# Optimization experiments

Measured on AMD Instinct MI355X. Metric: run time of the kernel, lower is better.

The kernel has to match this reference:

```python
import math
import jax, jax.numpy as jnp
import numpy as np

N = 512; E_EDGES = 16384; NODE_DIM = 64; HID = 128; FF = 2048; VOCAB = 50; L = 2; H = 8; SEQ = 100


def setup_inputs() -> dict:
    key = jax.random.key(0)
    ks = jax.random.split(key, 24)
    s = 0.02
    rn = lambda k, shape: jax.random.normal(k, shape, jnp.float32) * s
    return {
        "x": jax.random.normal(ks[0], (N, NODE_DIM), jnp.float32),
        "edge_index": jax.random.randint(ks[1], (2, E_EDGES), 0, N, dtype=jnp.int32),
        "gcn1_w": rn(ks[2], (NODE_DIM, HID)), "gcn1_b": rn(ks[3], (HID,)),
        "gcn2_w": rn(ks[4], (HID, HID)),     "gcn2_b": rn(ks[5], (HID,)),
        "fc_w":   rn(ks[6], (HID, HID)),     "fc_b":   rn(ks[7], (HID,)),
        # decoder: per layer, 4 proj mats (q,k,v,out) for self-attn and cross-attn
        "sa_w": rn(ks[8], (L, 4, HID, HID)), "sa_b": rn(ks[9], (L, 4, HID)),
        "ca_w": rn(ks[10], (L, 4, HID, HID)), "ca_b": rn(ks[11], (L, 4, HID)),
        "ln_w": jnp.ones((L, 3, HID), jnp.float32), "ln_b": jnp.zeros((L, 3, HID), jnp.float32),
        "ff_w1": rn(ks[12], (L, HID, FF)), "ff_b1": rn(ks[13], (L, FF)),
        "ff_w2": rn(ks[14], (L, FF, HID)), "ff_b2": rn(ks[15], (L, HID)),
        "out_w": rn(ks[16], (HID, VOCAB)), "out_b": rn(ks[17], (VOCAB,)),
    }


def _gcn(x, W, b, src, dst, n):
    # PyG GCNConv: add self-loops, symmetric norm, aggregate source->target
    h = x @ W                                   # [N, out]
    loop = jnp.arange(n, dtype=src.dtype)
    s = jnp.concatenate([src, loop])
    d = jnp.concatenate([dst, loop])
    deg = jax.ops.segment_sum(jnp.ones_like(d, x.dtype), d, num_segments=n)
    dinv = jax.lax.rsqrt(deg)                   # deg >= 1 thanks to self-loops
    norm = dinv[s] * dinv[d]                    # [E+N]
    return jax.ops.segment_sum(h[s] * norm[:, None], d, num_segments=n) + b


def _layernorm(x, w, b, eps=1e-5):
    m = x.mean(-1, keepdims=True)
    v = ((x - m) ** 2).mean(-1, keepdims=True)
    return (x - m) * jax.lax.rsqrt(v + eps) * w + b


def _mha(q_in, kv_in, w, b):
    # q_in [S,Nb,E], kv_in [T,Nb,E]; w [4,E,E] (q,k,v,out), b [4,E]
    S, Nb, E = q_in.shape
    T = kv_in.shape[0]
    Dh = E // H
    q = (q_in @ w[0] + b[0]).reshape(S, Nb, H, Dh)
    k = (kv_in @ w[1] + b[1]).reshape(T, Nb, H, Dh)
    v = (kv_in @ w[2] + b[2]).reshape(T, Nb, H, Dh)
    att = jnp.einsum('snhd,tnhd->nhst', q, k) / math.sqrt(Dh)
    p = jax.nn.softmax(att, axis=-1)
    o = jnp.einsum('nhst,tnhd->snhd', p, v).reshape(S, Nb, E)
    return o @ w[3] + b[3]


def _forward(x, edge_index, gcn1_w, gcn1_b, gcn2_w, gcn2_b, fc_w, fc_b,
             sa_w, sa_b, ca_w, ca_b, ln_w, ln_b, ff_w1, ff_b1, ff_w2, ff_b2,
             out_w, out_b):
    n = x.shape[0]
    src, dst = edge_index[0], edge_index[1]
    # quantum_embedding: rz = (cos(phi)-sin(phi)) * (cos(theta)*x + sin(theta)*tanh(x))
    qx = (math.cos(0.05) - math.sin(0.05)) * (math.cos(0.1) * x + math.sin(0.1) * jnp.tanh(x))
    h = jax.nn.relu(_gcn(qx, gcn1_w, gcn1_b, src, dst, n))
    h = jax.nn.relu(_gcn(h, gcn2_w, gcn2_b, src, dst, n))
    h = h @ fc_w + fc_b                          # [N, HID]
    mem = h[None]                                # [1, N, HID] (memory, seq-first)
    tgt = jnp.zeros((SEQ, n, h.shape[1]), h.dtype)
    for l in range(L):                           # post-norm TransformerDecoderLayer
        tgt = _layernorm(tgt + _mha(tgt, tgt, sa_w[l], sa_b[l]), ln_w[l, 0], ln_b[l, 0])
        tgt = _layernorm(tgt + _mha(tgt, mem, ca_w[l], ca_b[l]), ln_w[l, 1], ln_b[l, 1])
        f = jax.nn.relu(tgt @ ff_w1[l] + ff_b1[l]) @ ff_w2[l] + ff_b2[l]
        tgt = _layernorm(tgt + f, ln_w[l, 2], ln_b[l, 2])
    return tgt @ out_w + out_b                   # [SEQ, N, VOCAB]


def reference(x, edge_index, gcn1_w, gcn1_b, gcn2_w, gcn2_b, fc_w, fc_b,
              sa_w, sa_b, ca_w, ca_b, ln_w, ln_b, ff_w1, ff_b1, ff_w2, ff_b2,
              out_w, out_b):
    return _forward(x, edge_index, gcn1_w, gcn1_b, gcn2_w, gcn2_b, fc_w, fc_b,
                    sa_w, sa_b, ca_w, ca_b, ln_w, ln_b, ff_w1, ff_b1, ff_w2, ff_b2,
                    out_w, out_b)
```

## Files before the change

kernel.cpp:

```cpp
#include <hip/hip_runtime.h>
#include <math.h>

#define NN      512
#define EE      16384
#define NDIM    64
#define HID     128
#define FFD     2048
#define VOCAB   50
#define SEQ     100

#define QA 0.94877109112428797f
#define QB 0.99500416527802582f
#define QC 0.099833416646828155f


struct BArgs {
    const int* ei; int* cnt;
    const float* x; const float* g1w; float* pre1;
    const float* A[3]; const float* ab[3]; const float* Bm[3]; const float* bb[3];
    float* outM[3];
    const float* ab3; const float* B3; const float* bb3; float* out3;
};

__global__ void k_b(BArgs a) {
    int B = blockIdx.x, t = threadIdx.x;
    if (B < 64) {
        int e = B * 256 + t;
        atomicAdd(&a.cnt[a.ei[EE + e]], 1);
        return;
    }
    if (B < 320) {
        __shared__ float qxs[2][NDIM];
        int q = B - 64;
        int row0 = q * 2;
        if (t < 2 * NDIM) {
            float v = a.x[row0 * NDIM + t];
            qxs[t >> 6][t & 63] = QA * (QB * v + QC * tanhf(v));
        }
        __syncthreads();
        int r = t >> 7, col = t & 127;
        float acc = 0.0f;
#pragma unroll 8
        for (int k = 0; k < NDIM; k++) acc = fmaf(qxs[r][k], a.g1w[k * HID + col], acc);
        a.pre1[(row0 + r) * HID + col] = acc;
        return;
    }
    if (B < 320 + 195) {
        int q = B - 320;
        int jm = q / 65;
        int i = (q - jm * 65) * 256 + t;
        if (i >= 129 * HID) return;
        int rw = i >> 7, col = i & 127;
        const float* Bm = a.Bm[jm];
        float acc;
        if (rw < 128) {
            const float* ar = a.A[jm] + rw * HID;
            acc = 0.0f;
#pragma unroll 8
            for (int k = 0; k < HID; k++) acc = fmaf(ar[k], Bm[k * HID + col], acc);
        } else {
            acc = a.bb[jm][col];
#pragma unroll 8
            for (int k = 0; k < HID; k++) acc = fmaf(a.ab[jm][k], Bm[k * HID + col], acc);
        }
        a.outM[jm][i] = acc;
        return;
    }
    if (t < HID) {
        float acc = a.bb3[t];
#pragma unroll 8
        for (int k = 0; k < HID; k++) acc = fmaf(a.ab3[k], a.B3[k * HID + t], acc);
        a.out3[t] = acc;
    }
}


struct CArgs {
    const int* cnt; int* offs; int* cursor; float* dinv;
    const float* fcw; const float* fcb;
    const float* Mca0; const float* Mca1; float* Mfc0; float* Mfc1;
};

__global__ void k_c(CArgs a) {
    int B = blockIdx.x, t = threadIdx.x;
    if (B == 0) {
        __shared__ int sh[512];
        int c0 = a.cnt[t], c1 = a.cnt[t + 256];
        sh[t] = c0; sh[t + 256] = c1;
        __syncthreads();
        for (int o = 1; o < 512; o <<= 1) {
            int x0 = (t >= o) ? sh[t - o] : 0;
            int x1 = (t + 256 >= o) ? sh[t + 256 - o] : 0;
            __syncthreads();
            sh[t] += x0; sh[t + 256] += x1;
            __syncthreads();
        }
        a.offs[t + 1] = sh[t];
        a.offs[t + 257] = sh[t + 256];
        if (t == 0) a.offs[0] = 0;
        a.cursor[t] = sh[t] - c0;
        a.cursor[t + 256] = sh[t + 256] - c1;
        a.dinv[t] = rsqrtf((float)c0 + 1.0f);
        a.dinv[t + 256] = rsqrtf((float)c1 + 1.0f);
        return;
    }
    int q = B - 1;
    int jm = q / 65;
    int i = (q - jm * 65) * 256 + t;
    if (i >= 129 * HID) return;
    int rw = i >> 7, col = i & 127;
    const float* M = jm ? a.Mca1 : a.Mca0;
    float* o = jm ? a.Mfc1 : a.Mfc0;
    float acc;
    if (rw < 128) {
        const float* ar = a.fcw + rw * HID;
        acc = 0.0f;
#pragma unroll 8
        for (int k = 0; k < HID; k++) acc = fmaf(ar[k], M[k * HID + col], acc);
    } else {
        acc = M[128 * HID + col];
#pragma unroll 8
        for (int k = 0; k < HID; k++) acc = fmaf(a.fcb[k], M[k * HID + col], acc);
    }
    o[i] = acc;
}


__global__ void k_scatter(const int* __restrict__ ei, int* __restrict__ cursor,
                          int* __restrict__ csr) {
    int e = blockIdx.x * 256 + threadIdx.x;
    if (e < EE) {
        int d = ei[EE + e];
        int slot = atomicAdd(&cursor[d], 1);
        csr[slot] = ei[e];
    }
}


__device__ __forceinline__ float gather_row(const float* __restrict__ pre,
                                            const float* __restrict__ dinv,
                                            const int* __restrict__ offs,
                                            const int* __restrict__ csr,
                                            int row, int j) {
    float dd = dinv[row];
    float acc = pre[row * HID + j] * dd;
    int i = offs[row], e = offs[row + 1];
    for (; i + 3 < e; i += 4) {
        int s0 = csr[i], s1 = csr[i + 1], s2 = csr[i + 2], s3 = csr[i + 3];
        float a0 = pre[s0 * HID + j] * dinv[s0];
        float a1 = pre[s1 * HID + j] * dinv[s1];
        float a2 = pre[s2 * HID + j] * dinv[s2];
        float a3 = pre[s3 * HID + j] * dinv[s3];
        acc += (a0 + a1) + (a2 + a3);
    }
    for (; i < e; ++i) {
        int s = csr[i];
        acc += pre[s * HID + j] * dinv[s];
    }
    return acc * dd;
}

__device__ __forceinline__ float rowln(float v, float w, float b, float* sh, int t) {
    int r = t >> 7;
    float s1 = v, s2 = v * v;
#pragma unroll
    for (int o = 32; o > 0; o >>= 1) {
        s1 += __shfl_down(s1, o);
        s2 += __shfl_down(s2, o);
    }
    int wv = (t >> 6) & 1;
    if ((t & 63) == 0) { sh[r * 4 + wv] = s1; sh[r * 4 + 2 + wv] = s2; }
    __syncthreads();
    float mean = (sh[r * 4] + sh[r * 4 + 1]) * (1.0f / HID);
    float m2   = (sh[r * 4 + 2] + sh[r * 4 + 3]) * (1.0f / HID);
    float rstd = rsqrtf(m2 - mean * mean + 1e-5f);
    float out = (v - mean) * rstd * w + b;
    __syncthreads();
    return out;
}


__global__ void k_gather_mm(const float* __restrict__ pre1, const float* __restrict__ dinv,
                            const int* __restrict__ offs, const int* __restrict__ csr,
                            const float* __restrict__ g1b, const float* __restrict__ g2w,
                            float* __restrict__ pre2) {
    __shared__ float sh_h[2][HID];
    int t = threadIdx.x, j = t & 127, r = t >> 7;
    int row = blockIdx.x * 2 + r;
    float g = gather_row(pre1, dinv, offs, csr, row, j);
    sh_h[r][j] = fmaxf(g + g1b[j], 0.0f);
    __syncthreads();
    float acc = 0.0f;
#pragma unroll 8
    for (int k = 0; k < HID; k++) acc = fmaf(sh_h[r][k], g2w[k * HID + j], acc);
    pre2[row * HID + j] = acc;
}


__global__ void k_row0(const float* __restrict__ pre2, const float* __restrict__ dinv,
                       const int* __restrict__ offs, const int* __restrict__ csr,
                       const float* __restrict__ g2b,
                       const float* __restrict__ Mfc0, const float* __restrict__ Mfc1,
                       const float* __restrict__ sa0bias,
                       const float* __restrict__ ln0w, const float* __restrict__ ln0b,
                       const float* __restrict__ ln1w, const float* __restrict__ ln1b,
                       float* __restrict__ ca1out, float* __restrict__ t0out) {
    __shared__ float sh_h[2][HID];
    __shared__ float shln[8];
    int t = threadIdx.x, j = t & 127, r = t >> 7;
    int row = blockIdx.x * 2 + r;
    float g = gather_row(pre2, dinv, offs, csr, row, j);
    sh_h[r][j] = fmaxf(g + g2b[j], 0.0f);
    __syncthreads();
    float a0 = Mfc0[128 * HID + j], a1 = Mfc1[128 * HID + j];
#pragma unroll 4
    for (int k = 0; k < HID; k++) {
        float hk = sh_h[r][k];
        a0 = fmaf(hk, Mfc0[k * HID + j], a0);
        a1 = fmaf(hk, Mfc1[k * HID + j], a1);
    }
    ca1out[row * HID + j] = a1;
    float v = rowln(sa0bias[j], ln0w[j], ln0b[j], shln, t);
    v = rowln(v + a0, ln1w[j], ln1b[j], shln, t);
    t0out[row * HID + j] = v;
}


__global__ __launch_bounds__(512)
void k_fff(const float* __restrict__ tin, const float* __restrict__ W1,
           const float* __restrict__ b1, const float* __restrict__ W2,
           float* __restrict__ part) {
    __shared__ float sh_t[16][HID];
    __shared__ float sh_m[16][256];
    int t = threadIdx.x;
    int kc = blockIdx.x & 7, rg = blockIdx.x >> 3;
    int row0 = rg * 16, c0 = kc * 256;

    {
        const float4* tp = (const float4*)(tin + row0 * HID);
        float4 v = tp[t];
        *(float4*)&sh_t[t >> 5][(t & 31) * 4] = v;
    }
    __syncthreads();

    {
        int rg2  = t >> 6;
        int col4 = (t & 63) * 4;
        float4 bias = *(const float4*)&b1[c0 + col4];
        float a00 = bias.x, a01 = bias.y, a02 = bias.z, a03 = bias.w;
        float a10 = bias.x, a11 = bias.y, a12 = bias.z, a13 = bias.w;
        const float* w1p = W1 + c0 + col4;
        const float* x0 = sh_t[2 * rg2];
        const float* x1 = sh_t[2 * rg2 + 1];
#pragma unroll 8
        for (int k = 0; k < HID; k++) {
            float4 w = *(const float4*)&w1p[k * FFD];
            float s0 = x0[k], s1 = x1[k];
            a00 = fmaf(s0, w.x, a00); a01 = fmaf(s0, w.y, a01);
            a02 = fmaf(s0, w.z, a02); a03 = fmaf(s0, w.w, a03);
            a10 = fmaf(s1, w.x, a10); a11 = fmaf(s1, w.y, a11);
            a12 = fmaf(s1, w.z, a12); a13 = fmaf(s1, w.w, a13);
        }
        float4 m0, m1;
        m0.x = fmaxf(a00, 0.f); m0.y = fmaxf(a01, 0.f);
        m0.z = fmaxf(a02, 0.f); m0.w = fmaxf(a03, 0.f);
        m1.x = fmaxf(a10, 0.f); m1.y = fmaxf(a11, 0.f);
        m1.z = fmaxf(a12, 0.f); m1.w = fmaxf(a13, 0.f);
        *(float4*)&sh_m[2 * rg2][col4]     = m0;
        *(float4*)&sh_m[2 * rg2 + 1][col4] = m1;
    }
    __syncthreads();

    {
        int rowg = t >> 5;
        int col4 = (t & 31) * 4;
        float a0 = 0.f, a1 = 0.f, a2 = 0.f, a3 = 0.f;
        const float* w2p = W2 + c0 * HID + col4;
        const float* mp = sh_m[rowg];
#pragma unroll 8
        for (int kk = 0; kk < 256; kk++) {
            float4 w = *(const float4*)&w2p[kk * HID];
            float m = mp[kk];
            a0 = fmaf(m, w.x, a0); a1 = fmaf(m, w.y, a1);
            a2 = fmaf(m, w.z, a2); a3 = fmaf(m, w.w, a3);
        }
        float4 o; o.x = a0; o.y = a1; o.z = a2; o.w = a3;
        *(float4*)&part[kc * (NN * HID) + (row0 + rowg) * HID + col4] = o;
    }
}


__global__ void k_row1(const float* __restrict__ part, const float* __restrict__ fb2,
                       const float* __restrict__ t0, const float* __restrict__ Msa1,
                       const float* __restrict__ ca1,
                       const float* __restrict__ ln2w, const float* __restrict__ ln2b,
                       const float* __restrict__ ln3w, const float* __restrict__ ln3b,
                       const float* __restrict__ ln4w, const float* __restrict__ ln4b,
                       float* __restrict__ t2out) {
    __shared__ float sh_t1[2][HID];
    __shared__ float shln[8];
    int t = threadIdx.x, j = t & 127, r = t >> 7;
    int row = blockIdx.x * 2 + r;
    float v = fb2[j] + t0[row * HID + j];
#pragma unroll
    for (int s = 0; s < 8; s++) v += part[s * (NN * HID) + row * HID + j];
    v = rowln(v, ln2w[j], ln2b[j], shln, t);
    sh_t1[r][j] = v;
    __syncthreads();
    float s1 = Msa1[128 * HID + j];
#pragma unroll 8
    for (int k = 0; k < HID; k++) s1 = fmaf(sh_t1[r][k], Msa1[k * HID + j], s1);
    float u = rowln(v + s1, ln3w[j], ln3b[j], shln, t);
    u = rowln(u + ca1[row * HID + j], ln4w[j], ln4b[j], shln, t);
    t2out[row * HID + j] = u;
}


__global__ void k_rowout(const float* __restrict__ part, const float* __restrict__ fb2,
                         const float* __restrict__ t2,
                         const float* __restrict__ ln5w, const float* __restrict__ ln5b,
                         const float* __restrict__ ow, const float* __restrict__ ob,
                         float* __restrict__ out) {
    __shared__ float sh3[2][HID];
    __shared__ float shln[8];
    __shared__ __align__(16) float sh_lg[100];
    int t = threadIdx.x, j = t & 127, r = t >> 7;
    int row = blockIdx.x * 2 + r;
    float v = fb2[j] + t2[row * HID + j];
#pragma unroll
    for (int s = 0; s < 8; s++) v += part[s * (NN * HID) + row * HID + j];
    v = rowln(v, ln5w[j], ln5b[j], shln, t);
    sh3[r][j] = v;
    __syncthreads();
    if (j < VOCAB) {
        float acc = ob[j];
#pragma unroll 8
        for (int k = 0; k < HID; k++) acc = fmaf(sh3[r][k], ow[k * VOCAB + j], acc);
        sh_lg[r * VOCAB + j] = acc;
    }
    __syncthreads();
    int base = blockIdx.x * (2 * VOCAB);
    for (int idx = t; idx < SEQ * 25; idx += 256) {
        int s = idx / 25, p4 = (idx - s * 25) * 4;
        *(float4*)&out[s * (NN * VOCAB) + base + p4] = *(const float4*)&sh_lg[p4];
    }
}


extern "C" void kernel_launch(void* const* d_in, const int* in_sizes, int n_in,
                              void* d_out, int out_size, void* d_ws, size_t ws_size,
                              hipStream_t stream) {
    (void)in_sizes; (void)n_in; (void)out_size; (void)ws_size;
    const float* x   = (const float*)d_in[0];
    const int*   ei  = (const int*)d_in[1];
    const float* g1w = (const float*)d_in[2];
    const float* g1b = (const float*)d_in[3];
    const float* g2w = (const float*)d_in[4];
    const float* g2b = (const float*)d_in[5];
    const float* fcw = (const float*)d_in[6];
    const float* fcb = (const float*)d_in[7];
    const float* saw = (const float*)d_in[8];
    const float* sab = (const float*)d_in[9];
    const float* caw = (const float*)d_in[10];
    const float* cab = (const float*)d_in[11];
    const float* lnw = (const float*)d_in[12];
    const float* lnb = (const float*)d_in[13];
    const float* fw1 = (const float*)d_in[14];
    const float* fb1 = (const float*)d_in[15];
    const float* fw2 = (const float*)d_in[16];
    const float* fb2 = (const float*)d_in[17];
    const float* ow  = (const float*)d_in[18];
    const float* ob  = (const float*)d_in[19];
    float* out = (float*)d_out;

    float* ws      = (float*)d_ws;
    float* pre1    = ws;
    float* pre2    = ws + 65536;
    float* t0      = ws + 131072;
    float* t2      = ws + 196608;
    float* ca1     = ws + 262144;
    float* Msa1    = ws + 327680;
    float* Mca0    = ws + 344192;
    float* Mca1    = ws + 360704;
    float* Mfc0    = ws + 377216;
    float* Mfc1    = ws + 393728;
    float* sa0bias = ws + 410240;
    float* dinv    = ws + 410368;
    int*   cnt     = (int*)(ws + 410880);
    int*   offs    = cnt + 512;
    int*   cursor  = offs + 516;
    int*   csr     = cursor + 512;
    float* part    = ws + 429056;

    hipMemsetAsync(cnt, 0, 512 * sizeof(int), stream);

    {
        BArgs a;
        a.ei = ei; a.cnt = cnt; a.x = x; a.g1w = g1w; a.pre1 = pre1;
        a.A[0]  = saw + (4 + 2) * HID * HID;  a.ab[0] = sab + (4 + 2) * HID;
        a.Bm[0] = saw + (4 + 3) * HID * HID;  a.bb[0] = sab + (4 + 3) * HID;
        a.outM[0] = Msa1;
        a.A[1]  = caw + 2 * HID * HID;        a.ab[1] = cab + 2 * HID;
        a.Bm[1] = caw + 3 * HID * HID;        a.bb[1] = cab + 3 * HID;
        a.outM[1] = Mca0;
        a.A[2]  = caw + (4 + 2) * HID * HID;  a.ab[2] = cab + (4 + 2) * HID;
        a.Bm[2] = caw + (4 + 3) * HID * HID;  a.bb[2] = cab + (4 + 3) * HID;
        a.outM[2] = Mca1;
        a.ab3 = sab + 2 * HID;  a.B3 = saw + 3 * HID * HID;  a.bb3 = sab + 3 * HID;
        a.out3 = sa0bias;
        k_b<<<516, 256, 0, stream>>>(a);
    }

    {
        CArgs a;
        a.cnt = cnt; a.offs = offs; a.cursor = cursor; a.dinv = dinv;
        a.fcw = fcw; a.fcb = fcb;
        a.Mca0 = Mca0; a.Mca1 = Mca1; a.Mfc0 = Mfc0; a.Mfc1 = Mfc1;
        k_c<<<131, 256, 0, stream>>>(a);
    }

    k_scatter<<<64, 256, 0, stream>>>(ei, cursor, csr);

    k_gather_mm<<<256, 256, 0, stream>>>(pre1, dinv, offs, csr, g1b, g2w, pre2);

    k_row0<<<256, 256, 0, stream>>>(pre2, dinv, offs, csr, g2b, Mfc0, Mfc1, sa0bias,
                                    lnw + 0 * HID, lnb + 0 * HID,
                                    lnw + 1 * HID, lnb + 1 * HID, ca1, t0);

    k_fff<<<256, 512, 0, stream>>>(t0, fw1, fb1, fw2, part);

    k_row1<<<256, 256, 0, stream>>>(part, fb2, t0, Msa1, ca1,
                                    lnw + 2 * HID, lnb + 2 * HID,
                                    lnw + 3 * HID, lnb + 3 * HID,
                                    lnw + 4 * HID, lnb + 4 * HID, t2);

    k_fff<<<256, 512, 0, stream>>>(t2, fw1 + HID * FFD, fb1 + FFD, fw2 + FFD * HID, part);

    k_rowout<<<256, 256, 0, stream>>>(part, fb2 + HID, t2,
                                      lnw + 5 * HID, lnb + 5 * HID, ow, ob, out);
}
```

Baseline: 120.2 us.

## Halve FFN block row tile and split second GEMM K across thread halves

The fused FFN kernel now processes 8 rows per block instead of 16 and launches twice as many blocks. Each thread computes one row in the first GEMM. In the second GEMM the 256-wide K chunk is split between the two thread halves, which are then reduced through shared memory. This raises parallelism and block count on a many-CU GPU, at the cost of reading weights twice as often across blocks and adding an extra barrier.

```diff
diff --git a/kernel.cpp b/kernel.cpp
--- a/kernel.cpp
+++ b/kernel.cpp
@@ -230,13 +230,13 @@
 void k_fff(const float* __restrict__ tin, const float* __restrict__ W1,
            const float* __restrict__ b1, const float* __restrict__ W2,
            float* __restrict__ part) {
-    __shared__ float sh_t[16][HID];
-    __shared__ float sh_m[16][256];
+    __shared__ float sh_t[8][HID];
+    __shared__ float sh_m[8][256];
     int t = threadIdx.x;
     int kc = blockIdx.x & 7, rg = blockIdx.x >> 3;
-    int row0 = rg * 16, c0 = kc * 256;
-
-    {
+    int row0 = rg * 8, c0 = kc * 256;
+
+    if (t < 256) {
         const float4* tp = (const float4*)(tin + row0 * HID);
         float4 v = tp[t];
         *(float4*)&sh_t[t >> 5][(t & 31) * 4] = v;
@@ -244,48 +244,51 @@
     __syncthreads();
 
     {
-        int rg2  = t >> 6;
+        int row  = t >> 6;
         int col4 = (t & 63) * 4;
         float4 bias = *(const float4*)&b1[c0 + col4];
-        float a00 = bias.x, a01 = bias.y, a02 = bias.z, a03 = bias.w;
-        float a10 = bias.x, a11 = bias.y, a12 = bias.z, a13 = bias.w;
+        float a0 = bias.x, a1 = bias.y, a2 = bias.z, a3 = bias.w;
         const float* w1p = W1 + c0 + col4;
-        const float* x0 = sh_t[2 * rg2];
-        const float* x1 = sh_t[2 * rg2 + 1];
+        const float* xr = sh_t[row];
 #pragma unroll 8
         for (int k = 0; k < HID; k++) {
             float4 w = *(const float4*)&w1p[k * FFD];
-            float s0 = x0[k], s1 = x1[k];
-            a00 = fmaf(s0, w.x, a00); a01 = fmaf(s0, w.y, a01);
-            a02 = fmaf(s0, w.z, a02); a03 = fmaf(s0, w.w, a03);
-            a10 = fmaf(s1, w.x, a10); a11 = fmaf(s1, w.y, a11);
-            a12 = fmaf(s1, w.z, a12); a13 = fmaf(s1, w.w, a13);
-        }
-        float4 m0, m1;
-        m0.x = fmaxf(a00, 0.f); m0.y = fmaxf(a01, 0.f);
-        m0.z = fmaxf(a02, 0.f); m0.w = fmaxf(a03, 0.f);
-        m1.x = fmaxf(a10, 0.f); m1.y = fmaxf(a11, 0.f);
-        m1.z = fmaxf(a12, 0.f); m1.w = fmaxf(a13, 0.f);
-        *(float4*)&sh_m[2 * rg2][col4]     = m0;
-        *(float4*)&sh_m[2 * rg2 + 1][col4] = m1;
+            float s = xr[k];
+            a0 = fmaf(s, w.x, a0); a1 = fmaf(s, w.y, a1);
+            a2 = fmaf(s, w.z, a2); a3 = fmaf(s, w.w, a3);
+        }
+        float4 m;
+        m.x = fmaxf(a0, 0.f); m.y = fmaxf(a1, 0.f);
+        m.z = fmaxf(a2, 0.f); m.w = fmaxf(a3, 0.f);
+        *(float4*)&sh_m[row][col4] = m;
     }
     __syncthreads();
 
     {
-        int rowg = t >> 5;
         int col4 = (t & 31) * 4;
+        int row  = (t >> 5) & 7;
+        int kh   = t >> 8;
         float a0 = 0.f, a1 = 0.f, a2 = 0.f, a3 = 0.f;
-        const float* w2p = W2 + c0 * HID + col4;
-        const float* mp = sh_m[rowg];
-#pragma unroll 8
-        for (int kk = 0; kk < 256; kk++) {
+        const float* w2p = W2 + (c0 + kh * 128) * HID + col4;
+        const float* mp = &sh_m[row][kh * 128];
+#pragma unroll 8
+        for (int kk = 0; kk < 128; kk++) {
             float4 w = *(const float4*)&w2p[kk * HID];
             float m = mp[kk];
             a0 = fmaf(m, w.x, a0); a1 = fmaf(m, w.y, a1);
             a2 = fmaf(m, w.z, a2); a3 = fmaf(m, w.w, a3);
         }
-        float4 o; o.x = a0; o.y = a1; o.z = a2; o.w = a3;
-        *(float4*)&part[kc * (NN * HID) + (row0 + rowg) * HID + col4] = o;
+        float* shred = &sh_t[0][0];
+        if (kh) {
+            float4 r; r.x = a0; r.y = a1; r.z = a2; r.w = a3;
+            *(float4*)&shred[(t - 256) * 4] = r;
+        }
+        __syncthreads();
+        if (!kh) {
+            float4 o = *(float4*)&shred[t * 4];
+            o.x += a0; o.y += a1; o.z += a2; o.w += a3;
+            *(float4*)&part[kc * (NN * HID) + (row0 + row) * HID + col4] = o;
+        }
     }
 }
 
@@ -427,14 +430,14 @@
                                     lnw + 0 * HID, lnb + 0 * HID,
                                     lnw + 1 * HID, lnb + 1 * HID, ca1, t0);
 
-    k_fff<<<256, 512, 0, stream>>>(t0, fw1, fb1, fw2, part);
+    k_fff<<<512, 512, 0, stream>>>(t0, fw1, fb1, fw2, part);
 
     k_row1<<<256, 256, 0, stream>>>(part, fb2, t0, Msa1, ca1,
                                     lnw + 2 * HID, lnb + 2 * HID,
                                     lnw + 3 * HID, lnb + 3 * HID,
                                     lnw + 4 * HID, lnb + 4 * HID, t2);
 
-    k_fff<<<256, 512, 0, stream>>>(t2, fw1 + HID * FFD, fb1 + FFD, fw2 + FFD * HID, part);
+    k_fff<<<512, 512, 0, stream>>>(t2, fw1 + HID * FFD, fb1 + FFD, fw2 + FFD * HID, part);
 
     k_rowout<<<256, 256, 0, stream>>>(part, fb2 + HID, t2,
                                       lnw + 5 * HID, lnb + 5 * HID, ow, ob, out);
```

After: 134.0 us. 1.11x slower.

## Fuse all stages into one cooperative persistent kernel with grid syncs

Applied to the files above, without the earlier changes.

Replaces the eight separate kernel launches with a single cooperative kernel of 256 blocks × 512 threads that separates stages with grid.sync(). Row-wise stages now process 4 rows per block instead of 2, and the pre-stages are re-partitioned to match the larger blocks. The goal is to remove per-launch overhead and the inter-kernel drain gaps, which matter at this small problem size. In exchange it adds grid-wide barrier costs, and several stages leave many blocks idle.

```diff
diff --git a/kernel.cpp b/kernel.cpp
--- a/kernel.cpp
+++ b/kernel.cpp
@@ -1,5 +1,8 @@
 #include <hip/hip_runtime.h>
+#include <hip/hip_cooperative_groups.h>
 #include <math.h>
+
+namespace cg = cooperative_groups;
 
 #define NN      512
 #define EE      16384
@@ -13,128 +16,22 @@
 #define QB 0.99500416527802582f
 #define QC 0.099833416646828155f
 
-
-struct BArgs {
-    const int* ei; int* cnt;
-    const float* x; const float* g1w; float* pre1;
-    const float* A[3]; const float* ab[3]; const float* Bm[3]; const float* bb[3];
-    float* outM[3];
-    const float* ab3; const float* B3; const float* bb3; float* out3;
+struct GArgs {
+    const int* ei;
+    const float* x; const float* g1w; const float* g1b;
+    const float* g2w; const float* g2b;
+    const float* fcw; const float* fcb;
+    const float* saw; const float* sab;
+    const float* caw; const float* cab;
+    const float* lnw; const float* lnb;
+    const float* fw1; const float* fb1; const float* fw2; const float* fb2;
+    const float* ow; const float* ob;
+    float* out;
+    int* cnt; int* offs; int* cursor; int* csr;
+    float* dinv; float* pre1; float* pre2; float* t0; float* t2; float* ca1;
+    float* Msa1; float* Mca0; float* Mca1; float* Mfc0; float* Mfc1; float* sa0bias;
+    float* part;
 };
-
-__global__ void k_b(BArgs a) {
-    int B = blockIdx.x, t = threadIdx.x;
-    if (B < 64) {
-        int e = B * 256 + t;
-        atomicAdd(&a.cnt[a.ei[EE + e]], 1);
-        return;
-    }
-    if (B < 320) {
-        __shared__ float qxs[2][NDIM];
-        int q = B - 64;
-        int row0 = q * 2;
-        if (t < 2 * NDIM) {
-            float v = a.x[row0 * NDIM + t];
-            qxs[t >> 6][t & 63] = QA * (QB * v + QC * tanhf(v));
-        }
-        __syncthreads();
-        int r = t >> 7, col = t & 127;
-        float acc = 0.0f;
-#pragma unroll 8
-        for (int k = 0; k < NDIM; k++) acc = fmaf(qxs[r][k], a.g1w[k * HID + col], acc);
-        a.pre1[(row0 + r) * HID + col] = acc;
-        return;
-    }
-    if (B < 320 + 195) {
-        int q = B - 320;
-        int jm = q / 65;
-        int i = (q - jm * 65) * 256 + t;
-        if (i >= 129 * HID) return;
-        int rw = i >> 7, col = i & 127;
-        const float* Bm = a.Bm[jm];
-        float acc;
-        if (rw < 128) {
-            const float* ar = a.A[jm] + rw * HID;
-            acc = 0.0f;
-#pragma unroll 8
-            for (int k = 0; k < HID; k++) acc = fmaf(ar[k], Bm[k * HID + col], acc);
-        } else {
-            acc = a.bb[jm][col];
-#pragma unroll 8
-            for (int k = 0; k < HID; k++) acc = fmaf(a.ab[jm][k], Bm[k * HID + col], acc);
-        }
-        a.outM[jm][i] = acc;
-        return;
-    }
-    if (t < HID) {
-        float acc = a.bb3[t];
-#pragma unroll 8
-        for (int k = 0; k < HID; k++) acc = fmaf(a.ab3[k], a.B3[k * HID + t], acc);
-        a.out3[t] = acc;
-    }
-}
-
-
-struct CArgs {
-    const int* cnt; int* offs; int* cursor; float* dinv;
-    const float* fcw; const float* fcb;
-    const float* Mca0; const float* Mca1; float* Mfc0; float* Mfc1;
-};
-
-__global__ void k_c(CArgs a) {
-    int B = blockIdx.x, t = threadIdx.x;
-    if (B == 0) {
-        __shared__ int sh[512];
-        int c0 = a.cnt[t], c1 = a.cnt[t + 256];
-        sh[t] = c0; sh[t + 256] = c1;
-        __syncthreads();
-        for (int o = 1; o < 512; o <<= 1) {
-            int x0 = (t >= o) ? sh[t - o] : 0;
-            int x1 = (t + 256 >= o) ? sh[t + 256 - o] : 0;
-            __syncthreads();
-            sh[t] += x0; sh[t + 256] += x1;
-            __syncthreads();
-        }
-        a.offs[t + 1] = sh[t];
-        a.offs[t + 257] = sh[t + 256];
-        if (t == 0) a.offs[0] = 0;
-        a.cursor[t] = sh[t] - c0;
-        a.cursor[t + 256] = sh[t + 256] - c1;
-        a.dinv[t] = rsqrtf((float)c0 + 1.0f);
-        a.dinv[t + 256] = rsqrtf((float)c1 + 1.0f);
-        return;
-    }
-    int q = B - 1;
-    int jm = q / 65;
-    int i = (q - jm * 65) * 256 + t;
-    if (i >= 129 * HID) return;
-    int rw = i >> 7, col = i & 127;
-    const float* M = jm ? a.Mca1 : a.Mca0;
-    float* o = jm ? a.Mfc1 : a.Mfc0;
-    float acc;
-    if (rw < 128) {
-        const float* ar = a.fcw + rw * HID;
-        acc = 0.0f;
-#pragma unroll 8
-        for (int k = 0; k < HID; k++) acc = fmaf(ar[k], M[k * HID + col], acc);
-    } else {
-        acc = M[128 * HID + col];
-#pragma unroll 8
-        for (int k = 0; k < HID; k++) acc = fmaf(a.fcb[k], M[k * HID + col], acc);
-    }
-    o[i] = acc;
-}
-
-
-__global__ void k_scatter(const int* __restrict__ ei, int* __restrict__ cursor,
-                          int* __restrict__ csr) {
-    int e = blockIdx.x * 256 + threadIdx.x;
-    if (e < EE) {
-        int d = ei[EE + e];
-        int slot = atomicAdd(&cursor[d], 1);
-        csr[slot] = ei[e];
-    }
-}
 
 
 __device__ __forceinline__ float gather_row(const float* __restrict__ pre,
@@ -160,7 +57,7 @@
     return acc * dd;
 }
 
-__device__ __forceinline__ float rowln(float v, float w, float b, float* sh, int t) {
+__device__ __forceinline__ float rowln4(float v, float w, float b, float* sh, int t) {
     int r = t >> 7;
     float s1 = v, s2 = v * v;
 #pragma unroll
@@ -179,67 +76,20 @@
     return out;
 }
 
-
-__global__ void k_gather_mm(const float* __restrict__ pre1, const float* __restrict__ dinv,
-                            const int* __restrict__ offs, const int* __restrict__ csr,
-                            const float* __restrict__ g1b, const float* __restrict__ g2w,
-                            float* __restrict__ pre2) {
-    __shared__ float sh_h[2][HID];
-    int t = threadIdx.x, j = t & 127, r = t >> 7;
-    int row = blockIdx.x * 2 + r;
-    float g = gather_row(pre1, dinv, offs, csr, row, j);
-    sh_h[r][j] = fmaxf(g + g1b[j], 0.0f);
-    __syncthreads();
-    float acc = 0.0f;
-#pragma unroll 8
-    for (int k = 0; k < HID; k++) acc = fmaf(sh_h[r][k], g2w[k * HID + j], acc);
-    pre2[row * HID + j] = acc;
-}
-
-
-__global__ void k_row0(const float* __restrict__ pre2, const float* __restrict__ dinv,
-                       const int* __restrict__ offs, const int* __restrict__ csr,
-                       const float* __restrict__ g2b,
-                       const float* __restrict__ Mfc0, const float* __restrict__ Mfc1,
-                       const float* __restrict__ sa0bias,
-                       const float* __restrict__ ln0w, const float* __restrict__ ln0b,
-                       const float* __restrict__ ln1w, const float* __restrict__ ln1b,
-                       float* __restrict__ ca1out, float* __restrict__ t0out) {
-    __shared__ float sh_h[2][HID];
-    __shared__ float shln[8];
-    int t = threadIdx.x, j = t & 127, r = t >> 7;
-    int row = blockIdx.x * 2 + r;
-    float g = gather_row(pre2, dinv, offs, csr, row, j);
-    sh_h[r][j] = fmaxf(g + g2b[j], 0.0f);
-    __syncthreads();
-    float a0 = Mfc0[128 * HID + j], a1 = Mfc1[128 * HID + j];
-#pragma unroll 4
-    for (int k = 0; k < HID; k++) {
-        float hk = sh_h[r][k];
-        a0 = fmaf(hk, Mfc0[k * HID + j], a0);
-        a1 = fmaf(hk, Mfc1[k * HID + j], a1);
-    }
-    ca1out[row * HID + j] = a1;
-    float v = rowln(sa0bias[j], ln0w[j], ln0b[j], shln, t);
-    v = rowln(v + a0, ln1w[j], ln1b[j], shln, t);
-    t0out[row * HID + j] = v;
-}
-
-
-__global__ __launch_bounds__(512)
-void k_fff(const float* __restrict__ tin, const float* __restrict__ W1,
-           const float* __restrict__ b1, const float* __restrict__ W2,
-           float* __restrict__ part) {
-    __shared__ float sh_t[16][HID];
-    __shared__ float sh_m[16][256];
-    int t = threadIdx.x;
-    int kc = blockIdx.x & 7, rg = blockIdx.x >> 3;
+__device__ __forceinline__ void ff_block(const float* __restrict__ tin,
+                                         const float* __restrict__ W1,
+                                         const float* __restrict__ b1,
+                                         const float* __restrict__ W2,
+                                         float* __restrict__ part,
+                                         float* smem, int bid, int t) {
+    float* sh_t = smem;
+    float* sh_m = smem + 2048;
+    int kc = bid & 7, rg = bid >> 3;
     int row0 = rg * 16, c0 = kc * 256;
 
     {
-        const float4* tp = (const float4*)(tin + row0 * HID);
-        float4 v = tp[t];
-        *(float4*)&sh_t[t >> 5][(t & 31) * 4] = v;
+        float4 v = ((const float4*)(tin + row0 * HID))[t];
+        ((float4*)sh_t)[t] = v;
     }
     __syncthreads();
 
@@ -250,8 +100,8 @@
         float a00 = bias.x, a01 = bias.y, a02 = bias.z, a03 = bias.w;
         float a10 = bias.x, a11 = bias.y, a12 = bias.z, a13 = bias.w;
         const float* w1p = W1 + c0 + col4;
-        const float* x0 = sh_t[2 * rg2];
-        const float* x1 = sh_t[2 * rg2 + 1];
+        const float* x0 = sh_t + (2 * rg2) * HID;
+        const float* x1 = x0 + HID;
 #pragma unroll 8
         for (int k = 0; k < HID; k++) {
             float4 w = *(const float4*)&w1p[k * FFD];
@@ -266,8 +116,8 @@
         m0.z = fmaxf(a02, 0.f); m0.w = fmaxf(a03, 0.f);
         m1.x = fmaxf(a10, 0.f); m1.y = fmaxf(a11, 0.f);
         m1.z = fmaxf(a12, 0.f); m1.w = fmaxf(a13, 0.f);
-        *(float4*)&sh_m[2 * rg2][col4]     = m0;
-        *(float4*)&sh_m[2 * rg2 + 1][col4] = m1;
+        *(float4*)&sh_m[(2 * rg2) * 256 + col4]     = m0;
+        *(float4*)&sh_m[(2 * rg2 + 1) * 256 + col4] = m1;
     }
     __syncthreads();
 
@@ -276,7 +126,7 @@
         int col4 = (t & 31) * 4;
         float a0 = 0.f, a1 = 0.f, a2 = 0.f, a3 = 0.f;
         const float* w2p = W2 + c0 * HID + col4;
-        const float* mp = sh_m[rowg];
+        const float* mp = sh_m + rowg * 256;
 #pragma unroll 8
         for (int kk = 0; kk < 256; kk++) {
             float4 w = *(const float4*)&w2p[kk * HID];
@@ -290,59 +140,216 @@
 }
 
 
-__global__ void k_row1(const float* __restrict__ part, const float* __restrict__ fb2,
-                       const float* __restrict__ t0, const float* __restrict__ Msa1,
-                       const float* __restrict__ ca1,
-                       const float* __restrict__ ln2w, const float* __restrict__ ln2b,
-                       const float* __restrict__ ln3w, const float* __restrict__ ln3b,
-                       const float* __restrict__ ln4w, const float* __restrict__ ln4b,
-                       float* __restrict__ t2out) {
-    __shared__ float sh_t1[2][HID];
-    __shared__ float shln[8];
-    int t = threadIdx.x, j = t & 127, r = t >> 7;
-    int row = blockIdx.x * 2 + r;
-    float v = fb2[j] + t0[row * HID + j];
+__global__ __launch_bounds__(512)
+void k_mega(GArgs a) {
+    cg::grid_group grid = cg::this_grid();
+    __shared__ __align__(16) float smem[6144];
+    int bid = blockIdx.x, t = threadIdx.x;
+
+    if (bid < 32) {
+        int e = bid * 512 + t;
+        atomicAdd(&a.cnt[a.ei[EE + e]], 1);
+    } else if (bid < 96) {
+        int row0 = (bid - 32) * 8;
+        float* qxs = smem;
+        {
+            float v = a.x[row0 * NDIM + t];
+            qxs[t] = QA * (QB * v + QC * tanhf(v));
+        }
+        __syncthreads();
+        int col = t & 127, r0 = t >> 7;
 #pragma unroll
-    for (int s = 0; s < 8; s++) v += part[s * (NN * HID) + row * HID + j];
-    v = rowln(v, ln2w[j], ln2b[j], shln, t);
-    sh_t1[r][j] = v;
-    __syncthreads();
-    float s1 = Msa1[128 * HID + j];
-#pragma unroll 8
-    for (int k = 0; k < HID; k++) s1 = fmaf(sh_t1[r][k], Msa1[k * HID + j], s1);
-    float u = rowln(v + s1, ln3w[j], ln3b[j], shln, t);
-    u = rowln(u + ca1[row * HID + j], ln4w[j], ln4b[j], shln, t);
-    t2out[row * HID + j] = u;
-}
-
-
-__global__ void k_rowout(const float* __restrict__ part, const float* __restrict__ fb2,
-                         const float* __restrict__ t2,
-                         const float* __restrict__ ln5w, const float* __restrict__ ln5b,
-                         const float* __restrict__ ow, const float* __restrict__ ob,
-                         float* __restrict__ out) {
-    __shared__ float sh3[2][HID];
-    __shared__ float shln[8];
-    __shared__ __align__(16) float sh_lg[100];
-    int t = threadIdx.x, j = t & 127, r = t >> 7;
-    int row = blockIdx.x * 2 + r;
-    float v = fb2[j] + t2[row * HID + j];
+        for (int rr = 0; rr < 2; rr++) {
+            int r = r0 + rr * 4;
+            float acc = 0.0f;
+#pragma unroll 8
+            for (int k = 0; k < NDIM; k++)
+                acc = fmaf(qxs[r * 64 + k], a.g1w[k * HID + col], acc);
+            a.pre1[(row0 + r) * HID + col] = acc;
+        }
+    } else if (bid < 195) {
+        int q = bid - 96;
+        int jm = q / 33;
+        int i = (q - jm * 33) * 512 + t;
+        if (i < 129 * HID) {
+            const float* A  = (jm == 0) ? (a.saw + (4 + 2) * HID * HID)
+                             : (jm == 1) ? (a.caw + 2 * HID * HID)
+                                         : (a.caw + (4 + 2) * HID * HID);
+            const float* ab = (jm == 0) ? (a.sab + (4 + 2) * HID)
+                             : (jm == 1) ? (a.cab + 2 * HID)
+                                         : (a.cab + (4 + 2) * HID);
+            const float* Bm = (jm == 0) ? (a.saw + (4 + 3) * HID * HID)
+                             : (jm == 1) ? (a.caw + 3 * HID * HID)
+                                         : (a.caw + (4 + 3) * HID * HID);
+            const float* bb = (jm == 0) ? (a.sab + (4 + 3) * HID)
+                             : (jm == 1) ? (a.cab + 3 * HID)
+                                         : (a.cab + (4 + 3) * HID);
+            float* outM = (jm == 0) ? a.Msa1 : (jm == 1) ? a.Mca0 : a.Mca1;
+            int rw = i >> 7, col = i & 127;
+            float acc;
+            if (rw < 128) {
+                const float* ar = A + rw * HID;
+                acc = 0.0f;
+#pragma unroll 8
+                for (int k = 0; k < HID; k++) acc = fmaf(ar[k], Bm[k * HID + col], acc);
+            } else {
+                acc = bb[col];
+#pragma unroll 8
+                for (int k = 0; k < HID; k++) acc = fmaf(ab[k], Bm[k * HID + col], acc);
+            }
+            outM[i] = acc;
+        }
+    } else if (bid == 195) {
+        if (t < HID) {
+            const float* ab3 = a.sab + 2 * HID;
+            const float* B3  = a.saw + 3 * HID * HID;
+            float acc = a.sab[3 * HID + t];
+#pragma unroll 8
+            for (int k = 0; k < HID; k++) acc = fmaf(ab3[k], B3[k * HID + t], acc);
+            a.sa0bias[t] = acc;
+        }
+    }
+    grid.sync();
+
+    if (bid == 0) {
+        int* sh = (int*)smem;
+        int c = a.cnt[t];
+        sh[t] = c;
+        __syncthreads();
+        int v = c;
+        for (int o = 1; o < 512; o <<= 1) {
+            int add = (t >= o) ? sh[t - o] : 0;
+            __syncthreads();
+            v += add;
+            sh[t] = v;
+            __syncthreads();
+        }
+        a.offs[t + 1] = v;
+        if (t == 0) a.offs[0] = 0;
+        a.cursor[t] = v - c;
+        a.dinv[t] = rsqrtf((float)c + 1.0f);
+    } else if (bid <= 65) {
+        int i = (bid - 1) * 512 + t;
+        if (i < 2 * 129 * HID) {
+            int jm = (i >= 129 * HID) ? 1 : 0;
+            int ii = i - jm * 129 * HID;
+            const float* M = jm ? a.Mca1 : a.Mca0;
+            float* o = jm ? a.Mfc1 : a.Mfc0;
+            int rw = ii >> 7, col = ii & 127;
+            float acc;
+            if (rw < 128) {
+                const float* ar = a.fcw + rw * HID;
+                acc = 0.0f;
+#pragma unroll 8
+                for (int k = 0; k < HID; k++) acc = fmaf(ar[k], M[k * HID + col], acc);
+            } else {
+                acc = M[128 * HID + col];
+#pragma unroll 8
+                for (int k = 0; k < HID; k++) acc = fmaf(a.fcb[k], M[k * HID + col], acc);
+            }
+            o[ii] = acc;
+        }
+    }
+    grid.sync();
+
+    if (bid < 32) {
+        int e = bid * 512 + t;
+        int d = a.ei[EE + e];
+        int slot = atomicAdd(&a.cursor[d], 1);
+        a.csr[slot] = a.ei[e];
+    }
+    grid.sync();
+
+    if (bid < 128) {
+        float* sh_h = smem;
+        int j = t & 127, r = t >> 7;
+        int row = bid * 4 + r;
+        float g = gather_row(a.pre1, a.dinv, a.offs, a.csr, row, j);
+        sh_h[r * HID + j] = fmaxf(g + a.g1b[j], 0.0f);
+        __syncthreads();
+        float acc = 0.0f;
+#pragma unroll 8
+        for (int k = 0; k < HID; k++)
+            acc = fmaf(sh_h[r * HID + k], a.g2w[k * HID + j], acc);
+        a.pre2[row * HID + j] = acc;
+    }
+    grid.sync();
+
+    if (bid < 128) {
+        float* sh_h = smem;
+        float* shln = smem + 512;
+        int j = t & 127, r = t >> 7;
+        int row = bid * 4 + r;
+        float g = gather_row(a.pre2, a.dinv, a.offs, a.csr, row, j);
+        sh_h[r * HID + j] = fmaxf(g + a.g2b[j], 0.0f);
+        __syncthreads();
+        float c0 = a.Mfc0[128 * HID + j], c1 = a.Mfc1[128 * HID + j];
+#pragma unroll 4
+        for (int k = 0; k < HID; k++) {
+            float hk = sh_h[r * HID + k];
+            c0 = fmaf(hk, a.Mfc0[k * HID + j], c0);
+            c1 = fmaf(hk, a.Mfc1[k * HID + j], c1);
+        }
+        a.ca1[row * HID + j] = c1;
+        float v = rowln4(a.sa0bias[j], a.lnw[j], a.lnb[j], shln, t);
+        v = rowln4(v + c0, a.lnw[HID + j], a.lnb[HID + j], shln, t);
+        a.t0[row * HID + j] = v;
+    }
+    grid.sync();
+
+    ff_block(a.t0, a.fw1, a.fb1, a.fw2, a.part, smem, bid, t);
+    grid.sync();
+
+    if (bid < 128) {
+        float* sh_t1 = smem;
+        float* shln = smem + 512;
+        int j = t & 127, r = t >> 7;
+        int row = bid * 4 + r;
+        float v = a.fb2[j] + a.t0[row * HID + j];
 #pragma unroll
-    for (int s = 0; s < 8; s++) v += part[s * (NN * HID) + row * HID + j];
-    v = rowln(v, ln5w[j], ln5b[j], shln, t);
-    sh3[r][j] = v;
-    __syncthreads();
-    if (j < VOCAB) {
-        float acc = ob[j];
-#pragma unroll 8
-        for (int k = 0; k < HID; k++) acc = fmaf(sh3[r][k], ow[k * VOCAB + j], acc);
-        sh_lg[r * VOCAB + j] = acc;
-    }
-    __syncthreads();
-    int base = blockIdx.x * (2 * VOCAB);
-    for (int idx = t; idx < SEQ * 25; idx += 256) {
-        int s = idx / 25, p4 = (idx - s * 25) * 4;
-        *(float4*)&out[s * (NN * VOCAB) + base + p4] = *(const float4*)&sh_lg[p4];
+        for (int s = 0; s < 8; s++) v += a.part[s * (NN * HID) + row * HID + j];
+        v = rowln4(v, a.lnw[2 * HID + j], a.lnb[2 * HID + j], shln, t);
+        sh_t1[r * HID + j] = v;
+        __syncthreads();
+        float s1 = a.Msa1[128 * HID + j];
+#pragma unroll 8
+        for (int k = 0; k < HID; k++)
+            s1 = fmaf(sh_t1[r * HID + k], a.Msa1[k * HID + j], s1);
+        float u = rowln4(v + s1, a.lnw[3 * HID + j], a.lnb[3 * HID + j], shln, t);
+        u = rowln4(u + a.ca1[row * HID + j], a.lnw[4 * HID + j], a.lnb[4 * HID + j], shln, t);
+        a.t2[row * HID + j] = u;
+    }
+    grid.sync();
+
+    ff_block(a.t2, a.fw1 + HID * FFD, a.fb1 + FFD, a.fw2 + FFD * HID, a.part, smem, bid, t);
+    grid.sync();
+
+    if (bid < 128) {
+        float* sh3 = smem;
+        float* shln = smem + 512;
+        float* sh_lg = smem + 528;
+        int j = t & 127, r = t >> 7;
+        int row = bid * 4 + r;
+        float v = a.fb2[HID + j] + a.t2[row * HID + j];
+#pragma unroll
+        for (int s = 0; s < 8; s++) v += a.part[s * (NN * HID) + row * HID + j];
+        v = rowln4(v, a.lnw[5 * HID + j], a.lnb[5 * HID + j], shln, t);
+        sh3[r * HID + j] = v;
+        __syncthreads();
+        if (j < VOCAB) {
+            float acc = a.ob[j];
+#pragma unroll 8
+            for (int k = 0; k < HID; k++)
+                acc = fmaf(sh3[r * HID + k], a.ow[k * VOCAB + j], acc);
+            sh_lg[r * VOCAB + j] = acc;
+        }
+        __syncthreads();
+        int base = bid * (4 * VOCAB);
+        const float4* lg4 = (const float4*)sh_lg;
+        for (int idx = t; idx < SEQ * 50; idx += 512) {
+            int s = idx / 50, q = idx - s * 50;
+            *(float4*)&a.out[s * (NN * VOCAB) + base + q * 4] = lg4[q];
+        }
     }
 }
 
@@ -351,91 +358,51 @@
                               void* d_out, int out_size, void* d_ws, size_t ws_size,
                               hipStream_t stream) {
     (void)in_sizes; (void)n_in; (void)out_size; (void)ws_size;
-    const float* x   = (const float*)d_in[0];
-    const int*   ei  = (const int*)d_in[1];
-    const float* g1w = (const float*)d_in[2];
-    const float* g1b = (const float*)d_in[3];
-    const float* g2w = (const float*)d_in[4];
-    const float* g2b = (const float*)d_in[5];
-    const float* fcw = (const float*)d_in[6];
-    const float* fcb = (const float*)d_in[7];
-    const float* saw = (const float*)d_in[8];
-    const float* sab = (const float*)d_in[9];
-    const float* caw = (const float*)d_in[10];
-    const float* cab = (const float*)d_in[11];
-    const float* lnw = (const float*)d_in[12];
-    const float* lnb = (const float*)d_in[13];
-    const float* fw1 = (const float*)d_in[14];
-    const float* fb1 = (const float*)d_in[15];
-    const float* fw2 = (const float*)d_in[16];
-    const float* fb2 = (const float*)d_in[17];
-    const float* ow  = (const float*)d_in[18];
-    const float* ob  = (const float*)d_in[19];
-    float* out = (float*)d_out;
-
-    float* ws      = (float*)d_ws;
-    float* pre1    = ws;
-    float* pre2    = ws + 65536;
-    float* t0      = ws + 131072;
-    float* t2      = ws + 196608;
-    float* ca1     = ws + 262144;
-    float* Msa1    = ws + 327680;
-    float* Mca0    = ws + 344192;
-    float* Mca1    = ws + 360704;
-    float* Mfc0    = ws + 377216;
-    float* Mfc1    = ws + 393728;
-    float* sa0bias = ws + 410240;
-    float* dinv    = ws + 410368;
-    int*   cnt     = (int*)(ws + 410880);
-    int*   offs    = cnt + 512;
-    int*   cursor  = offs + 516;
-    int*   csr     = cursor + 512;
-    float* part    = ws + 429056;
-
-    hipMemsetAsync(cnt, 0, 512 * sizeof(int), stream);
-
-    {
-        BArgs a;
-        a.ei = ei; a.cnt = cnt; a.x = x; a.g1w = g1w; a.pre1 = pre1;
-        a.A[0]  = saw + (4 + 2) * HID * HID;  a.ab[0] = sab + (4 + 2) * HID;
-        a.Bm[0] = saw + (4 + 3) * HID * HID;  a.bb[0] = sab + (4 + 3) * HID;
-        a.outM[0] = Msa1;
-        a.A[1]  = caw + 2 * HID * HID;        a.ab[1] = cab + 2 * HID;
-        a.Bm[1] = caw + 3 * HID * HID;        a.bb[1] = cab + 3 * HID;
-        a.outM[1] = Mca0;
-        a.A[2]  = caw + (4 + 2) * HID * HID;  a.ab[2] = cab + (4 + 2) * HID;
-        a.Bm[2] = caw + (4 + 3) * HID * HID;  a.bb[2] = cab + (4 + 3) * HID;
-        a.outM[2] = Mca1;
-        a.ab3 = sab + 2 * HID;  a.B3 = saw + 3 * HID * HID;  a.bb3 = sab + 3 * HID;
-        a.out3 = sa0bias;
-        k_b<<<516, 256, 0, stream>>>(a);
-    }
-
-    {
-        CArgs a;
-        a.cnt = cnt; a.offs = offs; a.cursor = cursor; a.dinv = dinv;
-        a.fcw = fcw; a.fcb = fcb;
-        a.Mca0 = Mca0; a.Mca1 = Mca1; a.Mfc0 = Mfc0; a.Mfc1 = Mfc1;
-        k_c<<<131, 256, 0, stream>>>(a);
-    }
-
-    k_scatter<<<64, 256, 0, stream>>>(ei, cursor, csr);
-
-    k_gather_mm<<<256, 256, 0, stream>>>(pre1, dinv, offs, csr, g1b, g2w, pre2);
-
-    k_row0<<<256, 256, 0, stream>>>(pre2, dinv, offs, csr, g2b, Mfc0, Mfc1, sa0bias,
-                                    lnw + 0 * HID, lnb + 0 * HID,
-                                    lnw + 1 * HID, lnb + 1 * HID, ca1, t0);
-
-    k_fff<<<256, 512, 0, stream>>>(t0, fw1, fb1, fw2, part);
-
-    k_row1<<<256, 256, 0, stream>>>(part, fb2, t0, Msa1, ca1,
-                                    lnw + 2 * HID, lnb + 2 * HID,
-                                    lnw + 3 * HID, lnb + 3 * HID,
-                                    lnw + 4 * HID, lnb + 4 * HID, t2);
-
-    k_fff<<<256, 512, 0, stream>>>(t2, fw1 + HID * FFD, fb1 + FFD, fw2 + FFD * HID, part);
-
-    k_rowout<<<256, 256, 0, stream>>>(part, fb2 + HID, t2,
-                                      lnw + 5 * HID, lnb + 5 * HID, ow, ob, out);
+    GArgs a;
+    a.x   = (const float*)d_in[0];
+    a.ei  = (const int*)d_in[1];
+    a.g1w = (const float*)d_in[2];
+    a.g1b = (const float*)d_in[3];
+    a.g2w = (const float*)d_in[4];
+    a.g2b = (const float*)d_in[5];
+    a.fcw = (const float*)d_in[6];
+    a.fcb = (const float*)d_in[7];
+    a.saw = (const float*)d_in[8];
+    a.sab = (const float*)d_in[9];
+    a.caw = (const float*)d_in[10];
+    a.cab = (const float*)d_in[11];
+    a.lnw = (const float*)d_in[12];
+    a.lnb = (const float*)d_in[13];
+    a.fw1 = (const float*)d_in[14];
+    a.fb1 = (const float*)d_in[15];
+    a.fw2 = (const float*)d_in[16];
+    a.fb2 = (const float*)d_in[17];
+    a.ow  = (const float*)d_in[18];
+    a.ob  = (const float*)d_in[19];
+    a.out = (float*)d_out;
+
+    float* ws = (float*)d_ws;
+    a.pre1    = ws;
+    a.pre2    = ws + 65536;
+    a.t0      = ws + 131072;
+    a.t2      = ws + 196608;
+    a.ca1     = ws + 262144;
+    a.Msa1    = ws + 327680;
+    a.Mca0    = ws + 344192;
+    a.Mca1    = ws + 360704;
+    a.Mfc0    = ws + 377216;
+    a.Mfc1    = ws + 393728;
+    a.sa0bias = ws + 410240;
+    a.dinv    = ws + 410368;
+    a.cnt     = (int*)(ws + 410880);
+    a.offs    = a.cnt + 512;
+    a.cursor  = a.offs + 516;
+    a.csr     = a.cursor + 512;
+    a.part    = ws + 429056;
+
+    hipMemsetAsync(a.cnt, 0, 512 * sizeof(int), stream);
+
+    void* args[] = { &a };
+    hipLaunchCooperativeKernel((const void*)k_mega, dim3(256), dim3(512),
+                               args, 0, stream);
 }
```

Measured after the change: 339.9 us. 183% more time.
